# Optimization experiments

Hardware: AMD Instinct MI355X
Metric: run time of the kernel (lower is better)

Reference implementation:

```python
import jax, jax.numpy as jnp
import numpy as np

FEAT = 2048
NUM_CLASSES = 751
EPS = 1e-5


def setup_inputs() -> dict:
    key = jax.random.key(0)
    k1, k2, k3 = jax.random.split(key, 3)
    probe_x = jax.random.normal(k1, (64, FEAT), dtype=jnp.float32)
    gallery_x = jax.random.normal(k2, (256, FEAT), dtype=jnp.float32)
    # BatchNorm1d affine params (PyTorch init: gamma=1, beta=0)
    bn_gamma = jnp.ones((FEAT,), dtype=jnp.float32)
    bn_beta = jnp.zeros((FEAT,), dtype=jnp.float32)
    # classifier: weight ~ N(0, 0.001), bias = 0
    W = jax.random.normal(k3, (NUM_CLASSES, FEAT), dtype=jnp.float32) * 0.001
    b = jnp.zeros((NUM_CLASSES,), dtype=jnp.float32)
    return {"probe_x": probe_x, "gallery_x": gallery_x,
            "bn_gamma": bn_gamma, "bn_beta": bn_beta, "W": W, "b": b}


def reference(probe_x, gallery_x, bn_gamma, bn_beta, W, b):
    n_probe, feat = probe_x.shape
    n_gallery = gallery_x.shape[0]
    # broadcast squared difference: [Np, Ng, F]
    diff = jnp.square(probe_x[:, None, :] - gallery_x[None, :, :])
    d = diff.reshape(n_probe * n_gallery, feat)
    # BatchNorm1d in training mode: biased batch statistics over the batch dim
    mean = jnp.mean(d, axis=0)
    var = jnp.mean(jnp.square(d - mean), axis=0)
    bn = (d - mean) * (bn_gamma / jnp.sqrt(var + EPS)) + bn_beta
    # Linear classifier
    cls = jnp.einsum('nf,cf->nc', bn, W) + b
    return cls.reshape(n_probe, n_gallery, -1)
```

## Files before the change

kernel.cpp:

```cpp
#include <hip/hip_runtime.h>
#include <hip/hip_bf16.h>
#include <hip/hip_fp16.h>

#define FEAT 2048
#define NCLS 751
#define NPAD 768
#define NPRB 64
#define NGAL 256
#define WSCALE 256.0f

typedef _Float16 f16x8 __attribute__((ext_vector_type(8)));
typedef float f32x4 __attribute__((ext_vector_type(4)));

__device__ __forceinline__ unsigned short f2h_u(float x) {
  union { _Float16 h; unsigned short u; } v;
  v.h = (_Float16)x;
  return v.u;
}

__global__ void stats_kernel(const float* __restrict__ P, const float* __restrict__ G,
                             const float* __restrict__ gamma, const float* __restrict__ beta,
                             float* __restrict__ st) {
  int fx = threadIdx.x & 31, ry = threadIdx.x >> 5;
  int f = blockIdx.x * 32 + fx;
  float a1 = 0, a2 = 0, a3 = 0, a4 = 0;
  for (int r = ry; r < NPRB; r += 8) {
    float x = P[r * FEAT + f], x2 = x * x;
    a1 += x; a2 += x2; a3 += x2 * x; a4 += x2 * x2;
  }
  float b1 = 0, b2 = 0, b3 = 0, b4 = 0;
  for (int r = ry; r < NGAL; r += 8) {
    float x = G[r * FEAT + f], x2 = x * x;
    b1 += x; b2 += x2; b3 += x2 * x; b4 += x2 * x2;
  }
  __shared__ float red[8][8][32];
  float vals[8] = {a1, a2, a3, a4, b1, b2, b3, b4};
#pragma unroll
  for (int m = 0; m < 8; ++m) red[m][ry][fx] = vals[m];
  __syncthreads();
  if (ry == 0) {
    float mm[8];
#pragma unroll
    for (int m = 0; m < 8; ++m) {
      float sum = 0.f;
#pragma unroll
      for (int r = 0; r < 8; ++r) sum += red[m][r][fx];
      mm[m] = sum;
    }
    float M1p = mm[0] * (1.f / NPRB), M2p = mm[1] * (1.f / NPRB);
    float M3p = mm[2] * (1.f / NPRB), M4p = mm[3] * (1.f / NPRB);
    float M1g = mm[4] * (1.f / NGAL), M2g = mm[5] * (1.f / NGAL);
    float M3g = mm[6] * (1.f / NGAL), M4g = mm[7] * (1.f / NGAL);
    float mean = M2p - 2.f * M1p * M1g + M2g;
    float Ed2 = M4p - 4.f * M3p * M1g + 6.f * M2p * M2g - 4.f * M1p * M3g + M4g;
    float var = Ed2 - mean * mean;
    float sv = gamma[f] / sqrtf(var + 1e-5f);
    st[f] = sv;
    st[FEAT + f] = beta[f] - mean * sv;
  }
}

__global__ void prepw_kernel(const float* __restrict__ W, const float* __restrict__ b,
                             const float* __restrict__ st,
                             unsigned short* __restrict__ Wp, float* __restrict__ bp) {
  int c = blockIdx.x;
  int f = threadIdx.x * 8;
  float4 w0 = make_float4(0.f, 0.f, 0.f, 0.f), w1 = w0;
  if (c < NCLS) {
    const float4* wsrc = (const float4*)(W + (size_t)c * FEAT + f);
    w0 = wsrc[0]; w1 = wsrc[1];
  }
  const float4* s4 = (const float4*)(st + f);
  float4 s0 = s4[0], s1 = s4[1];
  const float4* t4 = (const float4*)(st + FEAT + f);
  float4 t0 = t4[0], t1 = t4[1];
  uint4 u;
  u.x = (unsigned int)f2h_u(w0.x * s0.x * WSCALE) | ((unsigned int)f2h_u(w0.y * s0.y * WSCALE) << 16);
  u.y = (unsigned int)f2h_u(w0.z * s0.z * WSCALE) | ((unsigned int)f2h_u(w0.w * s0.w * WSCALE) << 16);
  u.z = (unsigned int)f2h_u(w1.x * s1.x * WSCALE) | ((unsigned int)f2h_u(w1.y * s1.y * WSCALE) << 16);
  u.w = (unsigned int)f2h_u(w1.z * s1.z * WSCALE) | ((unsigned int)f2h_u(w1.w * s1.w * WSCALE) << 16);
  *(uint4*)(Wp + (size_t)c * FEAT + f) = u;
  float acc = t0.x * w0.x + t0.y * w0.y + t0.z * w0.z + t0.w * w0.w +
              t1.x * w1.x + t1.y * w1.y + t1.z * w1.z + t1.w * w1.w;
#pragma unroll
  for (int off = 32; off > 0; off >>= 1) acc += __shfl_down(acc, off, 64);
  __shared__ float r[4];
  int wave = threadIdx.x >> 6, lane = threadIdx.x & 63;
  if (lane == 0) r[wave] = acc;
  __syncthreads();
  if (threadIdx.x == 0) bp[c] = (c < NCLS ? b[c] : 0.f) + r[0] + r[1] + r[2] + r[3];
}

__global__ void agen_kernel(const float* __restrict__ P, const float* __restrict__ G,
                            unsigned short* __restrict__ A) {
  int n = blockIdx.x;
  int p = n >> 8, g = n & 255;
  int f = threadIdx.x * 8;
  const float4* p4 = (const float4*)(P + (size_t)p * FEAT + f);
  const float4* g4 = (const float4*)(G + (size_t)g * FEAT + f);
  float4 pa = p4[0], pb = p4[1];
  float4 ga = g4[0], gb = g4[1];
  float d0 = pa.x - ga.x, d1 = pa.y - ga.y, d2 = pa.z - ga.z, d3 = pa.w - ga.w;
  float d4 = pb.x - gb.x, d5 = pb.y - gb.y, d6 = pb.z - gb.z, d7 = pb.w - gb.w;
  uint4 u;
  u.x = (unsigned int)f2h_u(d0 * d0) | ((unsigned int)f2h_u(d1 * d1) << 16);
  u.y = (unsigned int)f2h_u(d2 * d2) | ((unsigned int)f2h_u(d3 * d3) << 16);
  u.z = (unsigned int)f2h_u(d4 * d4) | ((unsigned int)f2h_u(d5 * d5) << 16);
  u.w = (unsigned int)f2h_u(d6 * d6) | ((unsigned int)f2h_u(d7 * d7) << 16);
  *(uint4*)(A + (size_t)n * FEAT + f) = u;
}

__global__ __launch_bounds__(256, 3)
void gemm_mat_kernel(const unsigned short* __restrict__ A,
                     const unsigned short* __restrict__ Wp,
                     const float* __restrict__ bp, float* __restrict__ out) {
  __shared__ unsigned short As[128 * 64];
  __shared__ unsigned short Bs[128 * 64];

  const int tid = threadIdx.x;
  const int lane = tid & 63, wave = tid >> 6;
  const int mtile = blockIdx.x, ntile = blockIdx.y;

  const int srow = tid >> 3;
  const int sch = (tid & 7) ^ (srow & 7);
  const unsigned short* ag = A + (size_t)(mtile * 128 + srow) * FEAT + sch * 8;
  const unsigned short* bg = Wp + (size_t)(ntile * 128 + srow) * FEAT + sch * 8;
  char* alds = (char*)As + wave * 1024;
  char* blds = (char*)Bs + wave * 1024;

  f32x4 acc[4][4];
#pragma unroll
  for (int mi = 0; mi < 4; ++mi)
#pragma unroll
    for (int ni = 0; ni < 4; ++ni) acc[mi][ni] = (f32x4){0.f, 0.f, 0.f, 0.f};

  const int wm = (wave & 1) * 64, wn = (wave >> 1) * 64;
  const int frow = lane & 15, fsw = lane & 7, fk = lane >> 4;

  for (int k0 = 0; k0 < FEAT; k0 += 64) {
    __syncthreads();
#pragma unroll
    for (int j = 0; j < 4; ++j) {
      __builtin_amdgcn_global_load_lds(
          (const __attribute__((address_space(1))) void*)(ag + k0 + (size_t)j * 32 * FEAT),
          (__attribute__((address_space(3))) void*)(alds + j * 4096), 16, 0, 0);
      __builtin_amdgcn_global_load_lds(
          (const __attribute__((address_space(1))) void*)(bg + k0 + (size_t)j * 32 * FEAT),
          (__attribute__((address_space(3))) void*)(blds + j * 4096), 16, 0, 0);
    }
    __syncthreads();

#pragma unroll
    for (int kk = 0; kk < 2; ++kk) {
      const int slot = (kk * 4 + fk) ^ fsw;
      f16x8 af[4], bf[4];
#pragma unroll
      for (int mi = 0; mi < 4; ++mi)
        af[mi] = *(const f16x8*)(As + (wm + mi * 16 + frow) * 64 + slot * 8);
#pragma unroll
      for (int ni = 0; ni < 4; ++ni)
        bf[ni] = *(const f16x8*)(Bs + (wn + ni * 16 + frow) * 64 + slot * 8);
#pragma unroll
      for (int mi = 0; mi < 4; ++mi)
#pragma unroll
        for (int ni = 0; ni < 4; ++ni)
          acc[mi][ni] = __builtin_amdgcn_mfma_f32_16x16x32_f16(af[mi], bf[ni], acc[mi][ni], 0, 0, 0);
    }
  }

  const int col0 = ntile * 128 + wn + (lane & 15);
  const int row0 = mtile * 128 + wm + ((lane >> 4) << 2);
#pragma unroll
  for (int ni = 0; ni < 4; ++ni) {
    int col = col0 + ni * 16;
    if (col >= NCLS) continue;
    float bv = bp[col];
#pragma unroll
    for (int mi = 0; mi < 4; ++mi) {
      int row = row0 + mi * 16;
#pragma unroll
      for (int r = 0; r < 4; ++r)
        out[(size_t)(row + r) * NCLS + col] = acc[mi][ni][r] * (1.0f / WSCALE) + bv;
    }
  }
}

extern "C" void kernel_launch(void* const* d_in, const int* in_sizes, int n_in,
                              void* d_out, int out_size, void* d_ws, size_t ws_size,
                              hipStream_t stream) {
  const float* P = (const float*)d_in[0];
  const float* G = (const float*)d_in[1];
  const float* gamma = (const float*)d_in[2];
  const float* beta = (const float*)d_in[3];
  const float* W = (const float*)d_in[4];
  const float* b = (const float*)d_in[5];
  float* out = (float*)d_out;

  float* st = (float*)d_ws;
  float* bp = st + 2 * FEAT;
  unsigned short* Wp = (unsigned short*)(bp + NPAD);
  unsigned short* A = Wp + (size_t)NPAD * FEAT;

  hipLaunchKernelGGL(agen_kernel, dim3(NPRB * NGAL), dim3(256), 0, stream, P, G, A);
  hipLaunchKernelGGL(stats_kernel, dim3(64), dim3(256), 0, stream, P, G, gamma, beta, st);
  hipLaunchKernelGGL(prepw_kernel, dim3(NPAD), dim3(256), 0, stream, W, b, st, Wp, bp);
  hipLaunchKernelGGL(gemm_mat_kernel, dim3(128, 6), dim3(256), 0, stream, A, Wp, bp, out);
}
```

Measured before the change: 173.5 us.

## Fuse squared-difference A generation into GEMM main loop

Removes the separate kernel that materialised the fp16 squared-difference matrix in global memory. The GEMM now builds A tiles on the fly: the probe row is staged in LDS, gallery rows are register-prefetched one k-step ahead, and the fp16 squares are written into swizzled LDS. This avoids the 32 MB A write/read round-trip and one launch. In exchange it adds ALU and conversion work inside the GEMM loop, an extra barrier per iteration, higher register pressure from the prefetch buffers, and gallery data reread by every n-tile.

```diff
diff --git a/kernel.cpp b/kernel.cpp
--- a/kernel.cpp
+++ b/kernel.cpp
@@ -91,42 +91,38 @@
   if (threadIdx.x == 0) bp[c] = (c < NCLS ? b[c] : 0.f) + r[0] + r[1] + r[2] + r[3];
 }
 
-__global__ void agen_kernel(const float* __restrict__ P, const float* __restrict__ G,
-                            unsigned short* __restrict__ A) {
-  int n = blockIdx.x;
-  int p = n >> 8, g = n & 255;
-  int f = threadIdx.x * 8;
-  const float4* p4 = (const float4*)(P + (size_t)p * FEAT + f);
-  const float4* g4 = (const float4*)(G + (size_t)g * FEAT + f);
-  float4 pa = p4[0], pb = p4[1];
-  float4 ga = g4[0], gb = g4[1];
-  float d0 = pa.x - ga.x, d1 = pa.y - ga.y, d2 = pa.z - ga.z, d3 = pa.w - ga.w;
-  float d4 = pb.x - gb.x, d5 = pb.y - gb.y, d6 = pb.z - gb.z, d7 = pb.w - gb.w;
-  uint4 u;
-  u.x = (unsigned int)f2h_u(d0 * d0) | ((unsigned int)f2h_u(d1 * d1) << 16);
-  u.y = (unsigned int)f2h_u(d2 * d2) | ((unsigned int)f2h_u(d3 * d3) << 16);
-  u.z = (unsigned int)f2h_u(d4 * d4) | ((unsigned int)f2h_u(d5 * d5) << 16);
-  u.w = (unsigned int)f2h_u(d6 * d6) | ((unsigned int)f2h_u(d7 * d7) << 16);
-  *(uint4*)(A + (size_t)n * FEAT + f) = u;
-}
-
 __global__ __launch_bounds__(256, 3)
-void gemm_mat_kernel(const unsigned short* __restrict__ A,
-                     const unsigned short* __restrict__ Wp,
-                     const float* __restrict__ bp, float* __restrict__ out) {
+void gemm_fused_kernel(const float* __restrict__ P, const float* __restrict__ G,
+                       const unsigned short* __restrict__ Wp,
+                       const float* __restrict__ bp, float* __restrict__ out) {
   __shared__ unsigned short As[128 * 64];
   __shared__ unsigned short Bs[128 * 64];
+  __shared__ float Ps[FEAT];
 
   const int tid = threadIdx.x;
   const int lane = tid & 63, wave = tid >> 6;
   const int mtile = blockIdx.x, ntile = blockIdx.y;
+  const int p = mtile >> 1;
 
   const int srow = tid >> 3;
   const int sch = (tid & 7) ^ (srow & 7);
-  const unsigned short* ag = A + (size_t)(mtile * 128 + srow) * FEAT + sch * 8;
+  const float* gp = G + (size_t)((mtile & 1) * 128 + srow) * FEAT + sch * 8;
   const unsigned short* bg = Wp + (size_t)(ntile * 128 + srow) * FEAT + sch * 8;
-  char* alds = (char*)As + wave * 1024;
+  unsigned short* asw = As + srow * 64 + (tid & 7) * 8;
   char* blds = (char*)Bs + wave * 1024;
+
+  {
+    const float4* psrc = (const float4*)(P + (size_t)p * FEAT) + tid * 2;
+    float4 pa = psrc[0], pb = psrc[1];
+    float4* pd = (float4*)Ps + tid * 2;
+    pd[0] = pa; pd[1] = pb;
+  }
+  float4 g0[4], g1[4];
+#pragma unroll
+  for (int j = 0; j < 4; ++j) {
+    const float4* gs = (const float4*)(gp + (size_t)j * 32 * FEAT);
+    g0[j] = gs[0]; g1[j] = gs[1];
+  }
 
   f32x4 acc[4][4];
 #pragma unroll
@@ -137,18 +133,40 @@
   const int wm = (wave & 1) * 64, wn = (wave >> 1) * 64;
   const int frow = lane & 15, fsw = lane & 7, fk = lane >> 4;
 
+  __syncthreads();
+
   for (int k0 = 0; k0 < FEAT; k0 += 64) {
-    __syncthreads();
-#pragma unroll
-    for (int j = 0; j < 4; ++j) {
-      __builtin_amdgcn_global_load_lds(
-          (const __attribute__((address_space(1))) void*)(ag + k0 + (size_t)j * 32 * FEAT),
-          (__attribute__((address_space(3))) void*)(alds + j * 4096), 16, 0, 0);
+#pragma unroll
+    for (int j = 0; j < 4; ++j)
       __builtin_amdgcn_global_load_lds(
           (const __attribute__((address_space(1))) void*)(bg + k0 + (size_t)j * 32 * FEAT),
           (__attribute__((address_space(3))) void*)(blds + j * 4096), 16, 0, 0);
+
+    const float* pr = Ps + k0 + sch * 8;
+    float4 p0 = *(const float4*)pr;
+    float4 p1 = *(const float4*)(pr + 4);
+#pragma unroll
+    for (int j = 0; j < 4; ++j) {
+      float d0 = p0.x - g0[j].x, d1 = p0.y - g0[j].y;
+      float d2 = p0.z - g0[j].z, d3 = p0.w - g0[j].w;
+      float d4 = p1.x - g1[j].x, d5 = p1.y - g1[j].y;
+      float d6 = p1.z - g1[j].z, d7 = p1.w - g1[j].w;
+      uint4 u;
+      u.x = (unsigned int)f2h_u(d0 * d0) | ((unsigned int)f2h_u(d1 * d1) << 16);
+      u.y = (unsigned int)f2h_u(d2 * d2) | ((unsigned int)f2h_u(d3 * d3) << 16);
+      u.z = (unsigned int)f2h_u(d4 * d4) | ((unsigned int)f2h_u(d5 * d5) << 16);
+      u.w = (unsigned int)f2h_u(d6 * d6) | ((unsigned int)f2h_u(d7 * d7) << 16);
+      *(uint4*)(asw + j * 32 * 64) = u;
     }
     __syncthreads();
+
+    if (k0 + 64 < FEAT) {
+#pragma unroll
+      for (int j = 0; j < 4; ++j) {
+        const float4* gs = (const float4*)(gp + k0 + 64 + (size_t)j * 32 * FEAT);
+        g0[j] = gs[0]; g1[j] = gs[1];
+      }
+    }
 
 #pragma unroll
     for (int kk = 0; kk < 2; ++kk) {
@@ -166,6 +184,7 @@
         for (int ni = 0; ni < 4; ++ni)
           acc[mi][ni] = __builtin_amdgcn_mfma_f32_16x16x32_f16(af[mi], bf[ni], acc[mi][ni], 0, 0, 0);
     }
+    __syncthreads();
   }
 
   const int col0 = ntile * 128 + wn + (lane & 15);
@@ -199,10 +218,8 @@
   float* st = (float*)d_ws;
   float* bp = st + 2 * FEAT;
   unsigned short* Wp = (unsigned short*)(bp + NPAD);
-  unsigned short* A = Wp + (size_t)NPAD * FEAT;
-
-  hipLaunchKernelGGL(agen_kernel, dim3(NPRB * NGAL), dim3(256), 0, stream, P, G, A);
+
   hipLaunchKernelGGL(stats_kernel, dim3(64), dim3(256), 0, stream, P, G, gamma, beta, st);
   hipLaunchKernelGGL(prepw_kernel, dim3(NPAD), dim3(256), 0, stream, W, b, st, Wp, bp);
-  hipLaunchKernelGGL(gemm_mat_kernel, dim3(128, 6), dim3(256), 0, stream, A, Wp, bp, out);
-}
+  hipLaunchKernelGGL(gemm_fused_kernel, dim3(128, 6), dim3(256), 0, stream, P, G, Wp, bp, out);
+}
```

Result: no change. 173.0 us (-0.2%).
